# Performance work log

Hardware: AMD Instinct MI355X
Metric: run time of the kernel (lower is better)

## Reference

```python
import jax, jax.numpy as jnp
import numpy as np

B, S, D = 1024, 200, 128
NQ, NC, NQD, NCD = 50000, 1000, 101, 101


def _linear_params(k, fan_in, fan_out):
    bound = 1.0 / np.sqrt(fan_in)
    kw, kb = jax.random.split(k)
    W = jax.random.uniform(kw, (fan_out, fan_in), minval=-bound, maxval=bound, dtype=jnp.float32)
    b = jax.random.uniform(kb, (fan_out,), minval=-bound, maxval=bound, dtype=jnp.float32)
    return W, b


def setup_inputs() -> dict:
    key = jax.random.key(0)
    ks = jax.random.split(key, 17)
    Wx, bx = _linear_params(ks[0], 4 * D, D)
    Ws1, bs1 = _linear_params(ks[1], D, D)
    Ws2, bs2 = _linear_params(ks[2], D, D)
    Wp1, bp1 = _linear_params(ks[3], 2 * D, D)
    Wp2, bp2 = _linear_params(ks[4], 2 * D, D)
    Wk, bk = _linear_params(ks[5], 4 * D, D)
    Eq = jax.random.normal(ks[6], (NQ, D), dtype=jnp.float32)
    Ec = jax.random.normal(ks[7], (NC, D), dtype=jnp.float32)
    Eqd = jax.random.normal(ks[8], (NQD, D), dtype=jnp.float32)
    Ecd = jax.random.normal(ks[9], (NCD, D), dtype=jnp.float32)
    Ecorr = jax.random.normal(ks[10], (2, D), dtype=jnp.float32)
    # xavier_uniform init for h_pre (torch: gain*sqrt(6/(fan_in+fan_out)) on [B,D])
    bh = np.sqrt(6.0 / (B + D))
    h0 = jax.random.uniform(ks[11], (B, D), minval=-bh, maxval=bh, dtype=jnp.float32)
    question_seq = jax.random.randint(ks[12], (B, S), 0, NQ)
    concept_seq = jax.random.randint(ks[13], (B, S), 0, NC)
    question_diff_seq = jax.random.randint(ks[14], (B, S), 0, NQD)
    concept_diff_seq = jax.random.randint(ks[15], (B, S), 0, NCD)
    correct_seq = jax.random.randint(ks[16], (B, S), 0, 2)
    return dict(question_seq=question_seq, concept_seq=concept_seq,
                question_diff_seq=question_diff_seq, concept_diff_seq=concept_diff_seq,
                correct_seq=correct_seq,
                Eq=Eq, Ec=Ec, Eqd=Eqd, Ecd=Ecd, Ecorr=Ecorr,
                Wx=Wx, bx=bx, Ws1=Ws1, bs1=bs1, Ws2=Ws2, bs2=bs2,
                Wp1=Wp1, bp1=bp1, Wp2=Wp2, bp2=bp2, Wk=Wk, bk=bk, h0=h0)


def reference(question_seq, concept_seq, question_diff_seq, concept_diff_seq, correct_seq,
              Eq, Ec, Eqd, Ecd, Ecorr,
              Wx, bx, Ws1, bs1, Ws2, bs2, Wp1, bp1, Wp2, bp2, Wk, bk, h0):
    qe = Eq[question_seq]            # [B,S,D]
    ce = Ec[concept_seq]
    qde = Eqd[question_diff_seq]
    cde = Ecd[concept_diff_seq]
    corr = Ecorr[correct_seq]
    # generate_x_MLP applied to all timesteps at once (same math as per-step)
    x = jnp.concatenate([qe, ce, qde, cde], axis=-1) @ Wx.T + bx  # [B,S,D]
    # time-major inputs for the scan over t = 0 .. S-2
    xs = (jnp.swapaxes(x[:, :-1], 0, 1),      # x_t       [S-1,B,D]
          jnp.swapaxes(x[:, 1:], 0, 1),       # x_{t+1}
          jnp.swapaxes(corr[:, :-1], 0, 1),
          jnp.swapaxes(qde[:, :-1], 0, 1),
          jnp.swapaxes(cde[:, :-1], 0, 1))

    def step(h_pre, inp):
        xt, xnext, ct, qdt, cdt = inp
        s_in = xt - h_pre
        sdf = jax.nn.sigmoid(s_in @ Ws1.T + bs1) * jnp.tanh(s_in @ Ws2.T + bs2)  # dropout=eval identity
        p_in = jnp.concatenate([sdf, ct], axis=-1)
        pka = jax.nn.sigmoid(p_in @ Wp1.T + bp1) * jnp.tanh(p_in @ Wp2.T + bp2)
        k_in = jnp.concatenate([h_pre, ct, qdt, cdt], axis=-1)
        g = jax.nn.sigmoid(k_in @ Wk.T + bk)
        h = g * h_pre + (1.0 - g) * pka
        yt = jax.nn.sigmoid(jnp.sum(xnext * h, axis=-1))  # [B]
        return h, yt

    _, ys = jax.lax.scan(step, h0, xs)  # ys: [S-1,B]
    y = jnp.concatenate([ys.T, jnp.zeros((question_seq.shape[0], 1), x.dtype)], axis=1)  # [B,S], y[:, S-1]=0
    return y
```

## Files before the change

### kernel.cpp

```cpp
#include <hip/hip_runtime.h>
#include <hip/hip_bf16.h>


#define S_LEN 200
#define NBATCH 1024
#define DIM 128
#define LOG2E 1.4426950408889634f
#define NPROD 191

typedef short short8 __attribute__((ext_vector_type(8)));
typedef float f32x4 __attribute__((ext_vector_type(4)));

__device__ __forceinline__ unsigned short f2b(float f) {
  union { float f; unsigned u; } v; v.f = f;
  unsigned r = (v.u + 0x7FFFu + ((v.u >> 16) & 1u)) >> 16;
  return (unsigned short)r;
}
__device__ __forceinline__ float b2f(unsigned short b) {
  union { unsigned u; float f; } v; v.u = ((unsigned)b) << 16;
  return v.f;
}
__device__ __forceinline__ unsigned pk_bf16(float lo, float hi) {
  __hip_bfloat162 t = __float22bfloat162_rn(make_float2(lo, hi));
  union { __hip_bfloat162 h; unsigned u; } cv; cv.h = t;
  return cv.u;
}
__device__ __forceinline__ float fast_sigmoid(float x) {
  return __builtin_amdgcn_rcpf(1.0f + __builtin_amdgcn_exp2f(-LOG2E * x));
}
__device__ __forceinline__ float fast_tanh(float x) {
  return 2.0f * __builtin_amdgcn_rcpf(1.0f + __builtin_amdgcn_exp2f(-2.0f * LOG2E * x)) - 1.0f;
}
__device__ __forceinline__ void wg_barrier_lds() {
  __asm__ volatile("s_waitcnt lgkmcnt(0)\n\ts_barrier" ::: "memory");
}

__global__ void proj_all_kernel(const float* __restrict__ Eq, const float* __restrict__ Ec,
                                const float* __restrict__ Eqd, const float* __restrict__ Ecd,
                                const float* __restrict__ Ecorr,
                                const float* __restrict__ Wx,
                                const float* __restrict__ Wp1, const float* __restrict__ bp1,
                                const float* __restrict__ Wp2, const float* __restrict__ bp2,
                                const float* __restrict__ Wk, const float* __restrict__ bk,
                                unsigned short* __restrict__ Tq, unsigned short* __restrict__ Tc,
                                unsigned short* __restrict__ Tqd, unsigned short* __restrict__ Tcd,
                                unsigned short* __restrict__ Tkqd, unsigned short* __restrict__ Tkcd,
                                float* __restrict__ Tkc, float* __restrict__ Tp1c,
                                float* __restrict__ Tp2c, int* __restrict__ syncz) {
  const int bid = blockIdx.x;
  const int tid = threadIdx.x;
  if (bid >= 802) {
    const int blk = bid - 802;
    if (blk < 101) {
      const int o = tid & 127, half = tid >> 7;
      const float* e = (half ? Ecd : Eqd) + (size_t)blk * DIM;
      const float* wr = Wk + (size_t)o * 512 + (half ? 384 : 256);
      float a = 0.f;
      for (int k = 0; k < DIM; ++k) a = fmaf(e[k], wr[k], a);
      (half ? Tkcd : Tkqd)[blk * DIM + o] = f2b(a);
    } else {
      for (int idx = tid; idx < 768; idx += 256) {
        const int t = idx >> 8, e = (idx >> 7) & 1, o = idx & 127;
        const float* ec = Ecorr + e * DIM;
        const float* wr; float bias; float* dst;
        if (t == 0)      { wr = Wp1 + (size_t)o * 256 + 128; bias = bp1[o]; dst = Tp1c; }
        else if (t == 1) { wr = Wp2 + (size_t)o * 256 + 128; bias = bp2[o]; dst = Tp2c; }
        else             { wr = Wk  + (size_t)o * 512 + 128; bias = bk[o];  dst = Tkc;  }
        float a = bias;
        for (int k = 0; k < DIM; ++k) a = fmaf(ec[k], wr[k], a);
        dst[e * DIM + o] = a;
      }
      for (int i2 = tid; i2 < 272; i2 += 256) syncz[i2] = 0;
    }
    return;
  }
  const float* E; int M, coff, r0; unsigned short* T;
  if (bid < 782)      { E = Eq;  M = 50000; coff = 0;   T = Tq;  r0 = bid * 64; }
  else if (bid < 798) { E = Ec;  M = 1000;  coff = 128; T = Tc;  r0 = (bid - 782) * 64; }
  else if (bid < 800) { E = Eqd; M = 101;   coff = 256; T = Tqd; r0 = (bid - 798) * 64; }
  else                { E = Ecd; M = 101;   coff = 384; T = Tcd; r0 = (bid - 800) * 64; }

  __shared__ __align__(16) unsigned short A[64][136];
  {
    const int row = tid >> 2, cb = (tid & 3) * 32;
    union U8 { uint4 v; unsigned short s[8]; } o;
#pragma unroll
    for (int cc = 0; cc < 4; ++cc) {
      const int c8 = cb + cc * 8;
      if (r0 + row < M) {
        const float4 e0 = *(const float4*)(E + (size_t)(r0 + row) * DIM + c8);
        const float4 e1 = *(const float4*)(E + (size_t)(r0 + row) * DIM + c8 + 4);
        o.s[0] = f2b(e0.x); o.s[1] = f2b(e0.y); o.s[2] = f2b(e0.z); o.s[3] = f2b(e0.w);
        o.s[4] = f2b(e1.x); o.s[5] = f2b(e1.y); o.s[6] = f2b(e1.z); o.s[7] = f2b(e1.w);
      } else {
        o.v = make_uint4(0, 0, 0, 0);
      }
      *(uint4*)&A[row][c8] = o.v;
    }
  }
  __syncthreads();
  const int w = tid >> 6, L = tid & 63, q = L >> 4, m = L & 15;
  short8 bf[2][4];
#pragma unroll
  for (int T2 = 0; T2 < 2; ++T2) {
    const int n = 32 * w + 16 * T2 + m;
#pragma unroll
    for (int kb = 0; kb < 4; ++kb) {
      const float* src = Wx + (size_t)n * 512 + coff + kb * 32 + q * 8;
      const float4 v0 = *(const float4*)src;
      const float4 v1 = *(const float4*)(src + 4);
      short8 f;
      f[0] = (short)f2b(v0.x); f[1] = (short)f2b(v0.y);
      f[2] = (short)f2b(v0.z); f[3] = (short)f2b(v0.w);
      f[4] = (short)f2b(v1.x); f[5] = (short)f2b(v1.y);
      f[6] = (short)f2b(v1.z); f[7] = (short)f2b(v1.w);
      bf[T2][kb] = f;
    }
  }
  const f32x4 vzero = {0.f, 0.f, 0.f, 0.f};
#pragma unroll
  for (int mt = 0; mt < 4; ++mt) {
    short8 af[4];
#pragma unroll
    for (int kb = 0; kb < 4; ++kb) af[kb] = *(const short8*)&A[mt * 16 + m][kb * 32 + q * 8];
    f32x4 acc[2] = {vzero, vzero};
#pragma unroll
    for (int kb = 0; kb < 4; ++kb) {
#pragma unroll
      for (int T2 = 0; T2 < 2; ++T2)
        acc[T2] = __builtin_amdgcn_mfma_f32_16x16x32_bf16(af[kb], bf[T2][kb], acc[T2], 0, 0, 0);
    }
#pragma unroll
    for (int T2 = 0; T2 < 2; ++T2) {
      const int col = 32 * w + 16 * T2 + m;
#pragma unroll
      for (int i = 0; i < 4; ++i) {
        const int r = r0 + mt * 16 + q * 4 + i;
        if (r < M) T[(size_t)r * DIM + col] = f2b(acc[T2][i]);
      }
    }
  }
}

__global__ void build_x_kernel(const int* __restrict__ qs, const int* __restrict__ cs,
                               const int* __restrict__ qds, const int* __restrict__ cds,
                               const int* __restrict__ corr,
                               const unsigned short* __restrict__ Tq, const unsigned short* __restrict__ Tc,
                               const unsigned short* __restrict__ Tqd, const unsigned short* __restrict__ Tcd,
                               const float* __restrict__ bx, unsigned short* __restrict__ xg,
                               float* __restrict__ SSg, float* __restrict__ corrf) {
  const int r = blockIdx.x * 16 + (threadIdx.x >> 4);
  const int c8 = (threadIdx.x & 15) * 8;
  const int s = r >> 10, b = r & 1023;
  const int q = qs[b * S_LEN + s], c = cs[b * S_LEN + s];
  const int qd = qds[b * S_LEN + s], cd = cds[b * S_LEN + s];
  union U8 { uint4 v; unsigned short s[8]; };
  U8 vq, vc, vd, ve, o;
  vq.v = *(const uint4*)(Tq + (size_t)q * DIM + c8);
  vc.v = *(const uint4*)(Tc + (size_t)c * DIM + c8);
  vd.v = *(const uint4*)(Tqd + (size_t)qd * DIM + c8);
  ve.v = *(const uint4*)(Tcd + (size_t)cd * DIM + c8);
  const float4 bx0 = *(const float4*)(bx + c8);
  const float4 bx1 = *(const float4*)(bx + c8 + 4);
  float bb[8] = {bx0.x, bx0.y, bx0.z, bx0.w, bx1.x, bx1.y, bx1.z, bx1.w};
  float part = 0.f;
#pragma unroll
  for (int j = 0; j < 8; ++j) {
    const float sv = b2f(vq.s[j]) + b2f(vc.s[j]) + b2f(vd.s[j]) + b2f(ve.s[j]) + bb[j];
    o.s[j] = f2b(sv);
    const float xr = b2f(o.s[j]);
    part = fmaf(xr, xr, part);
  }
  *(uint4*)(xg + (size_t)r * DIM + c8) = o.v;
#pragma unroll
  for (int off = 1; off <= 8; off <<= 1) part += __shfl_xor(part, off, 64);
  if ((threadIdx.x & 15) == 0) {
    SSg[r] = part;
    corrf[r] = (float)corr[b * S_LEN + s];
  }
}

__global__ void gemm_xg_kernel(const unsigned short* __restrict__ xg,
                               const float* __restrict__ Wk,
                               const int* __restrict__ corr, const int* __restrict__ qds,
                               const int* __restrict__ cds,
                               const float* __restrict__ Tkc,
                               const unsigned short* __restrict__ Tkqd,
                               const unsigned short* __restrict__ Tkcd,
                               unsigned short* __restrict__ GG) {
  const int tid = threadIdx.x;
  const int r0 = blockIdx.x * 64;
  __shared__ __align__(16) unsigned short TS[64][136];
  {
    const int row = tid >> 2, cb = (tid & 3) * 32;
    const int r = r0 + row, t = r >> 10, b = r & 1023;
    const int ci = corr[b * S_LEN + t], qi = qds[b * S_LEN + t], di = cds[b * S_LEN + t];
    union U8 { uint4 v; unsigned short s[8]; };
#pragma unroll
    for (int cc = 0; cc < 4; ++cc) {
      const int c8 = cb + cc * 8;
      U8 vq, vc, o;
      vq.v = *(const uint4*)(Tkqd + (size_t)qi * DIM + c8);
      vc.v = *(const uint4*)(Tkcd + (size_t)di * DIM + c8);
      const float4 k0 = *(const float4*)(Tkc + (size_t)ci * DIM + c8);
      const float4 k1 = *(const float4*)(Tkc + (size_t)ci * DIM + c8 + 4);
      float kk[8] = {k0.x, k0.y, k0.z, k0.w, k1.x, k1.y, k1.z, k1.w};
#pragma unroll
      for (int j = 0; j < 8; ++j) o.s[j] = f2b(kk[j] + b2f(vq.s[j]) + b2f(vc.s[j]));
      *(uint4*)&TS[row][c8] = o.v;
    }
  }
  __syncthreads();
  const int w = tid >> 6, L = tid & 63, q = L >> 4, m = L & 15;
  short8 wk[2][4];
#pragma unroll
  for (int T = 0; T < 2; ++T) {
    const int n = 32 * w + 16 * T + m;
#pragma unroll
    for (int kb = 0; kb < 4; ++kb) {
      const float* src = Wk + (size_t)n * 512 + kb * 32 + q * 8;
      const float4 v0 = *(const float4*)src;
      const float4 v1 = *(const float4*)(src + 4);
      short8 f;
      f[0] = (short)f2b(v0.x); f[1] = (short)f2b(v0.y);
      f[2] = (short)f2b(v0.z); f[3] = (short)f2b(v0.w);
      f[4] = (short)f2b(v1.x); f[5] = (short)f2b(v1.y);
      f[6] = (short)f2b(v1.z); f[7] = (short)f2b(v1.w);
      wk[T][kb] = f;
    }
  }
  const f32x4 vzero = {0.f, 0.f, 0.f, 0.f};
#pragma unroll
  for (int mt = 0; mt < 4; ++mt) {
    short8 af[4];
#pragma unroll
    for (int kb = 0; kb < 4; ++kb)
      af[kb] = *(const short8*)(xg + (size_t)(r0 + mt * 16 + m) * DIM + kb * 32 + q * 8);
    f32x4 acc[2] = {vzero, vzero};
#pragma unroll
    for (int kb = 0; kb < 4; ++kb) {
#pragma unroll
      for (int T = 0; T < 2; ++T)
        acc[T] = __builtin_amdgcn_mfma_f32_16x16x32_bf16(af[kb], wk[T][kb], acc[T], 0, 0, 0);
    }
#pragma unroll
    for (int T = 0; T < 2; ++T) {
      const int col = 32 * w + 16 * T + m;
#pragma unroll
      for (int i = 0; i < 4; ++i) {
        const int row64 = mt * 16 + q * 4 + i;
        GG[(size_t)(r0 + row64) * DIM + col] = f2b(acc[T][i] + b2f(TS[row64][col]));
      }
    }
  }
}

__device__ __forceinline__ void producer_body(
    const int p,
    const int* __restrict__ qs, const int* __restrict__ cs,
    const int* __restrict__ qds, const int* __restrict__ cds,
    const int* __restrict__ corr,
    const unsigned short* __restrict__ Tq, const unsigned short* __restrict__ Tc,
    const unsigned short* __restrict__ Tqd, const unsigned short* __restrict__ Tcd,
    const float* __restrict__ bx, const float* __restrict__ Wk,
    const float* __restrict__ Tkc, const unsigned short* __restrict__ Tkqd,
    const unsigned short* __restrict__ Tkcd,
    unsigned short* __restrict__ X, unsigned short* __restrict__ GG,
    float* __restrict__ SSg, float* __restrict__ corrf,
    int* donecnt, unsigned short (*xtile)[136], unsigned short (*TS)[136]) {
  const int tid = threadIdx.x;
  const int w = tid >> 6, L = tid & 63, q = L >> 4, m = L & 15;
  const int n = 16 * w + m;
  short8 wk[4];
#pragma unroll
  for (int kb = 0; kb < 4; ++kb) {
    const float* src = Wk + (size_t)n * 512 + kb * 32 + q * 8;
    const float4 v0 = *(const float4*)src;
    const float4 v1 = *(const float4*)(src + 4);
    short8 f;
    f[0] = (short)f2b(v0.x); f[1] = (short)f2b(v0.y);
    f[2] = (short)f2b(v0.z); f[3] = (short)f2b(v0.w);
    f[4] = (short)f2b(v1.x); f[5] = (short)f2b(v1.y);
    f[6] = (short)f2b(v1.z); f[7] = (short)f2b(v1.w);
    wk[kb] = f;
  }
  const int row = tid >> 3, k8 = tid & 7;
  const int c0 = k8 * 16;
  float bxv[16];
#pragma unroll
  for (int j = 0; j < 4; ++j) {
    const float4 bv = *(const float4*)(bx + c0 + j * 4);
    bxv[4 * j + 0] = bv.x; bxv[4 * j + 1] = bv.y;
    bxv[4 * j + 2] = bv.z; bxv[4 * j + 3] = bv.w;
  }
  const f32x4 vzero = {0.f, 0.f, 0.f, 0.f};
  union U8 { uint4 v; unsigned short s[8]; };

  for (int i = p; i < 3200; i += NPROD) {
    const int t = i >> 4, c = i & 15;
    const int b = c * 64 + row;
    const int base = b * S_LEN + t;
    const int qi = qs[base], ci = cs[base], qdi = qds[base], cdi = cds[base], cri = corr[base];
    float part = 0.f;
#pragma unroll
    for (int jj = 0; jj < 2; ++jj) {
      const int c8 = c0 + jj * 8;
      U8 vq, vc, vd, ve, o;
      vq.v = *(const uint4*)(Tq + (size_t)qi * DIM + c8);
      vc.v = *(const uint4*)(Tc + (size_t)ci * DIM + c8);
      vd.v = *(const uint4*)(Tqd + (size_t)qdi * DIM + c8);
      ve.v = *(const uint4*)(Tcd + (size_t)cdi * DIM + c8);
#pragma unroll
      for (int j = 0; j < 8; ++j) {
        const float sv = b2f(vq.s[j]) + b2f(vc.s[j]) + b2f(vd.s[j]) + b2f(ve.s[j]) + bxv[jj * 8 + j];
        o.s[j] = f2b(sv);
        const float xr = b2f(o.s[j]);
        part = fmaf(xr, xr, part);
      }
      *(uint4*)&xtile[row][c8] = o.v;
      *(uint4*)(X + (size_t)(t * 1024 + b) * DIM + c8) = o.v;
    }
#pragma unroll
    for (int off2 = 1; off2 <= 4; off2 <<= 1) part += __shfl_xor(part, off2, 64);
    if (k8 == 0) {
      SSg[t * 1024 + b] = part;
      corrf[t * 1024 + b] = (float)cri;
    }
    if (t < 199) {
#pragma unroll
      for (int jj = 0; jj < 2; ++jj) {
        const int c8 = c0 + jj * 8;
        U8 vq, vc, o;
        vq.v = *(const uint4*)(Tkqd + (size_t)qdi * DIM + c8);
        vc.v = *(const uint4*)(Tkcd + (size_t)cdi * DIM + c8);
        const float4 k0 = *(const float4*)(Tkc + (size_t)cri * DIM + c8);
        const float4 k1 = *(const float4*)(Tkc + (size_t)cri * DIM + c8 + 4);
        float kk[8] = {k0.x, k0.y, k0.z, k0.w, k1.x, k1.y, k1.z, k1.w};
#pragma unroll
        for (int j = 0; j < 8; ++j) o.s[j] = f2b(kk[j] + b2f(vq.s[j]) + b2f(vc.s[j]));
        *(uint4*)&TS[row][c8] = o.v;
      }
    }
    __syncthreads();
    if (t < 199) {
#pragma unroll
      for (int mt = 0; mt < 4; ++mt) {
        short8 af[4];
#pragma unroll
        for (int kb = 0; kb < 4; ++kb) af[kb] = *(const short8*)&xtile[mt * 16 + m][kb * 32 + q * 8];
        f32x4 acc = vzero;
#pragma unroll
        for (int kb = 0; kb < 4; ++kb)
          acc = __builtin_amdgcn_mfma_f32_16x16x32_bf16(af[kb], wk[kb], acc, 0, 0, 0);
#pragma unroll
        for (int i2 = 0; i2 < 4; ++i2) {
          const int row64 = mt * 16 + q * 4 + i2;
          GG[(size_t)(t * 1024 + c * 64 + row64) * DIM + n] = f2b(acc[i2] + b2f(TS[row64][n]));
        }
      }
    }
    __syncthreads();
    if (tid == 0)
      __hip_atomic_fetch_add(donecnt + t, 1, __ATOMIC_RELEASE, __HIP_MEMORY_SCOPE_AGENT);
  }
}

template <bool PIPE>
__device__ __forceinline__ void scan_body(
    const unsigned short* __restrict__ xg, const unsigned short* __restrict__ gg,
    const float* __restrict__ SSg, const float* __restrict__ corrf,
    const float* __restrict__ h0,
    const float* __restrict__ Ws1, const float* __restrict__ bs1,
    const float* __restrict__ Ws2, const float* __restrict__ bs2,
    const float* __restrict__ Wp1, const float* __restrict__ Wp2,
    const float* __restrict__ Wk,
    const float* __restrict__ gTp1c, const float* __restrict__ gTp2c,
    float* __restrict__ outp, int* wmp, unsigned short* ldsbase) {
  unsigned short (*Sbuf)[136] = (unsigned short (*)[136])ldsbase;
  unsigned short (*Pbuf)[136] = (unsigned short (*)[136])(ldsbase + 16 * 136);

  const int tid = threadIdx.x;
  const int w = tid >> 6, L = tid & 63, q = L >> 4, m = L & 15;
  const int col16 = 16 * w + m;
  const int rbase = blockIdx.x << 4;
  const size_t SB = (size_t)NBATCH * DIM;

  short8 wf[5][4];
  {
    const float* Wptr[5] = {Ws1, Ws2, Wp1, Wp2, Wk};
    const int ldw[5] = {128, 128, 256, 256, 512};
#pragma unroll
    for (int M = 0; M < 5; ++M) {
#pragma unroll
      for (int kb = 0; kb < 4; ++kb) {
        const float* src = Wptr[M] + (size_t)col16 * ldw[M] + kb * 32 + q * 8;
        const float4 v0 = *(const float4*)src;
        const float4 v1 = *(const float4*)(src + 4);
        short8 f;
        f[0] = (short)f2b(v0.x); f[1] = (short)f2b(v0.y);
        f[2] = (short)f2b(v0.z); f[3] = (short)f2b(v0.w);
        f[4] = (short)f2b(v1.x); f[5] = (short)f2b(v1.y);
        f[6] = (short)f2b(v1.z); f[7] = (short)f2b(v1.w);
        wf[M][kb] = f;
      }
    }
  }
  const float bs1v = bs1[col16], bs2v = bs2[col16];
  const float tp1v0 = gTp1c[col16], dtp1 = gTp1c[DIM + col16] - tp1v0;
  const float tp2v0 = gTp2c[col16], dtp2 = gTp2c[DIM + col16] - tp2v0;
  if (tid < 16) outp[(size_t)(rbase + tid) * S_LEN + (S_LEN - 1)] = 0.0f;

  int wm_seen = 0;
  auto wait_wm = [&](int need) {
    if (wm_seen >= need) return;
    while (__hip_atomic_load(wmp, __ATOMIC_RELAXED, __HIP_MEMORY_SCOPE_AGENT) < need)
      __builtin_amdgcn_s_sleep(8);
    wm_seen = __hip_atomic_load(wmp, __ATOMIC_ACQUIRE, __HIP_MEMORY_SCOPE_AGENT);
  };
  if (PIPE) wait_wm(3);

  float h[4];
#pragma unroll
  for (int i = 0; i < 4; ++i) {
    const int b = rbase + q * 4 + i;
    const float hv = h0[(size_t)b * DIM + col16];
    h[i] = hv;
    const float xt = b2f(xg[(size_t)b * DIM + col16]);
    Sbuf[q * 4 + i][col16] = f2b(xt - hv);
  }
  float* poy = outp + (size_t)(rbase + m) * S_LEN;

  unsigned short XPA[4], XPB[4], GPA[4], GPB[4];
  float4 CFA, CFB;
  short8 XFA[4], XFB[4];
  float SSA, SSB;
  const unsigned short* pxA = xg + 3 * SB + (size_t)(rbase + q * 4) * DIM + col16;
  const unsigned short* pxB = pxA + SB;
  const unsigned short* pgA = gg + 2 * SB + (size_t)(rbase + q * 4) * DIM + col16;
  const unsigned short* pgB = pgA + SB;
  const float* pcA = corrf + 2 * NBATCH + rbase + q * 4;
  const float* pcB = pcA + NBATCH;
  const unsigned short* pfA = xg + 2 * SB + (size_t)(rbase + m) * DIM + q * 8;
  const unsigned short* pfB = pfA + SB;
  const float* psA = SSg + 2 * NBATCH + rbase + m;
  const float* psB = psA + NBATCH;
#pragma unroll
  for (int i = 0; i < 4; ++i) {
    XPA[i] = xg[SB + (size_t)(rbase + q * 4 + i) * DIM + col16];
    XPB[i] = xg[2 * SB + (size_t)(rbase + q * 4 + i) * DIM + col16];
    GPA[i] = gg[(size_t)(rbase + q * 4 + i) * DIM + col16];
    GPB[i] = gg[SB + (size_t)(rbase + q * 4 + i) * DIM + col16];
  }
  CFA = *(const float4*)(corrf + rbase + q * 4);
  CFB = *(const float4*)(corrf + NBATCH + rbase + q * 4);
#pragma unroll
  for (int kb = 0; kb < 4; ++kb) {
    XFA[kb] = *(const short8*)(xg + (size_t)(rbase + m) * DIM + kb * 32 + q * 8);
    XFB[kb] = *(const short8*)(xg + SB + (size_t)(rbase + m) * DIM + kb * 32 + q * 8);
  }
  SSA = SSg[rbase + m];
  SSB = SSg[NBATCH + rbase + m];

  const f32x4 vzero = {0.f, 0.f, 0.f, 0.f};

#define STEP(TCUR, XP, GP, CF, PX, PG, PC, XF, SSR, PF, PS)                    \
  do {                                                                         \
    const int t_ = (TCUR);                                                     \
    float xnv[4], ggv[4], cfv[4];                                              \
    _Pragma("unroll") for (int i = 0; i < 4; ++i) {                            \
      xnv[i] = b2f(XP[i]); ggv[i] = b2f(GP[i]);                                \
    }                                                                          \
    cfv[0] = CF.x; cfv[1] = CF.y; cfv[2] = CF.z; cfv[3] = CF.w;                \
    short8 xfr[4]; float ssv = SSR;                                            \
    if (w == 0) {                                                              \
      _Pragma("unroll") for (int kb = 0; kb < 4; ++kb) xfr[kb] = XF[kb];       \
    }                                                                          \
    _Pragma("unroll") for (int i = 0; i < 4; ++i) {                            \
      XP[i] = PX[i * DIM]; GP[i] = PG[i * DIM];                                \
    }                                                                          \
    CF = *(const float4*)PC;                                                   \
    PX += 2 * SB; PG += 2 * SB; PC += 2 * NBATCH;                              \
    if (w == 0) {                                                              \
      _Pragma("unroll") for (int kb = 0; kb < 4; ++kb)                         \
        XF[kb] = *(const short8*)(PF + kb * 32);                               \
      SSR = *PS;                                                               \
      PF += 2 * SB; PS += 2 * NBATCH;                                          \
    }                                                                          \
    wg_barrier_lds();                                       \
    short8 sf[4];                                                              \
    _Pragma("unroll") for (int kb = 0; kb < 4; ++kb)                           \
        sf[kb] = *(const short8*)&Sbuf[m][kb * 32 + q * 8];                    \
    f32x4 a1 = vzero, a2 = vzero, c1 = vzero;                                  \
    _Pragma("unroll") for (int kb = 0; kb < 4; ++kb) {                         \
      a1 = __builtin_amdgcn_mfma_f32_16x16x32_bf16(sf[kb], wf[0][kb], a1, 0, 0, 0); \
      a2 = __builtin_amdgcn_mfma_f32_16x16x32_bf16(sf[kb], wf[1][kb], a2, 0, 0, 0); \
      c1 = __builtin_amdgcn_mfma_f32_16x16x32_bf16(sf[kb], wf[4][kb], c1, 0, 0, 0); \
    }                                                                          \
    if (w == 0) {                                                              \
      f32x4 dt = vzero;                                                        \
      _Pragma("unroll") for (int kb = 0; kb < 4; ++kb)                         \
        dt = __builtin_amdgcn_mfma_f32_16x16x32_bf16(sf[kb], xfr[kb], dt, 0, 0, 0); \
      if (t_ > 0 && q == (m >> 2)) {                                           \
        const int ii = m & 3;                                                  \
        const float D = ii == 0 ? dt[0] : ii == 1 ? dt[1] : ii == 2 ? dt[2] : dt[3]; \
        poy[t_ - 1] = fast_sigmoid(ssv - D);                                   \
      }                                                                        \
    }                                                                          \
    _Pragma("unroll") for (int i2 = 0; i2 < 2; ++i2) {                         \
      const float s0 = fast_sigmoid(a1[2 * i2] + bs1v) * fast_tanh(a2[2 * i2] + bs2v); \
      const float s1 = fast_sigmoid(a1[2 * i2 + 1] + bs1v) * fast_tanh(a2[2 * i2 + 1] + bs2v); \
      const unsigned u = pk_bf16(s0, s1);                                      \
      Pbuf[q * 4 + 2 * i2][col16] = (unsigned short)u;                         \
      Pbuf[q * 4 + 2 * i2 + 1][col16] = (unsigned short)(u >> 16);             \
    }                                                                          \
    wg_barrier_lds();                                          \
    short8 pf[4];                                                              \
    _Pragma("unroll") for (int kb = 0; kb < 4; ++kb)                           \
        pf[kb] = *(const short8*)&Pbuf[m][kb * 32 + q * 8];                    \
    f32x4 p1 = vzero, p2 = vzero;                                              \
    _Pragma("unroll") for (int kb = 0; kb < 4; ++kb) {                         \
      p1 = __builtin_amdgcn_mfma_f32_16x16x32_bf16(pf[kb], wf[2][kb], p1, 0, 0, 0); \
      p2 = __builtin_amdgcn_mfma_f32_16x16x32_bf16(pf[kb], wf[3][kb], p2, 0, 0, 0); \
    }                                                                          \
    float sn[4];                                                               \
    _Pragma("unroll") for (int i = 0; i < 4; ++i) {                            \
      const float g = fast_sigmoid(ggv[i] - c1[i]);                            \
      const float t1v = fmaf(cfv[i], dtp1, tp1v0);                             \
      const float t2v = fmaf(cfv[i], dtp2, tp2v0);                             \
      const float pka = fast_sigmoid(p1[i] + t1v) * fast_tanh(p2[i] + t2v);    \
      const float hn = pka + g * (h[i] - pka);                                 \
      h[i] = hn;                                                               \
      sn[i] = xnv[i] - hn;                                                     \
    }                                                                          \
    _Pragma("unroll") for (int i2 = 0; i2 < 2; ++i2) {                         \
      const unsigned u = pk_bf16(sn[2 * i2], sn[2 * i2 + 1]);                  \
      Sbuf[q * 4 + 2 * i2][col16] = (unsigned short)u;                         \
      Sbuf[q * 4 + 2 * i2 + 1][col16] = (unsigned short)(u >> 16);             \
    }                                                                          \
  } while (0)

  for (int t2 = 0; t2 < 198; t2 += 2) {
    if (PIPE) {
      const int need = (t2 + 5 > 200) ? 200 : t2 + 5;
      wait_wm(need);
    }
    STEP(t2, XPA, GPA, CFA, pxA, pgA, pcA, XFA, SSA, pfA, psA);
    STEP(t2 + 1, XPB, GPB, CFB, pxB, pgB, pcB, XFB, SSB, pfB, psB);
  }
  STEP(198, XPA, GPA, CFA, pxA, pgA, pcA, XFA, SSA, pfA, psA);
#undef STEP

  wg_barrier_lds();
  if (w == 0) {
    short8 sf[4];
#pragma unroll
    for (int kb = 0; kb < 4; ++kb) sf[kb] = *(const short8*)&Sbuf[m][kb * 32 + q * 8];
    f32x4 dt = vzero;
#pragma unroll
    for (int kb = 0; kb < 4; ++kb)
      dt = __builtin_amdgcn_mfma_f32_16x16x32_bf16(sf[kb], XFB[kb], dt, 0, 0, 0);
    if (q == (m >> 2)) {
      const int ii = m & 3;
      const float D = ii == 0 ? dt[0] : ii == 1 ? dt[1] : ii == 2 ? dt[2] : dt[3];
      poy[S_LEN - 2] = fast_sigmoid(SSB - D);
    }
  }
}

template <bool PIPE>
__global__ __launch_bounds__(512, 2) void scan_fused_kernel(
    const unsigned short* __restrict__ xg, const unsigned short* __restrict__ gg,
    const float* __restrict__ SSg, const float* __restrict__ corrf,
    const float* __restrict__ h0,
    const float* __restrict__ Ws1, const float* __restrict__ bs1,
    const float* __restrict__ Ws2, const float* __restrict__ bs2,
    const float* __restrict__ Wp1, const float* __restrict__ Wp2,
    const float* __restrict__ WkF,
    const float* __restrict__ gTp1c, const float* __restrict__ gTp2c,
    float* __restrict__ outp,
    const int* __restrict__ qs, const int* __restrict__ cs,
    const int* __restrict__ qds, const int* __restrict__ cds,
    const int* __restrict__ corr,
    const unsigned short* __restrict__ Tq, const unsigned short* __restrict__ Tc,
    const unsigned short* __restrict__ Tqd, const unsigned short* __restrict__ Tcd,
    const float* __restrict__ bx, const float* __restrict__ Tkc,
    const unsigned short* __restrict__ Tkqd, const unsigned short* __restrict__ Tkcd,
    unsigned short* __restrict__ Xw, unsigned short* __restrict__ GGw,
    float* __restrict__ SSw, float* __restrict__ corrw,
    int* donecnt, int* wmp) {
  __shared__ __align__(16) unsigned short lds[PIPE ? 2 * 64 * 136 : 2 * 16 * 136];
  if (!PIPE || blockIdx.x < 64) {
    scan_body<PIPE>(xg, gg, SSg, corrf, h0, Ws1, bs1, Ws2, bs2, Wp1, Wp2, WkF,
                    gTp1c, gTp2c, outp, wmp, lds);
    return;
  }
  if constexpr (PIPE) {
    if (blockIdx.x == 255) {
      if (threadIdx.x == 0) {
        for (int t = 0; t < S_LEN; ++t) {
          while (__hip_atomic_load(donecnt + t, __ATOMIC_RELAXED, __HIP_MEMORY_SCOPE_AGENT) < 16)
            __builtin_amdgcn_s_sleep(8);
          (void)__hip_atomic_load(donecnt + t, __ATOMIC_ACQUIRE, __HIP_MEMORY_SCOPE_AGENT);
          __hip_atomic_store(wmp, t + 1, __ATOMIC_RELEASE, __HIP_MEMORY_SCOPE_AGENT);
        }
      }
      return;
    }
    producer_body(blockIdx.x - 64, qs, cs, qds, cds, corr, Tq, Tc, Tqd, Tcd, bx,
                  WkF, Tkc, Tkqd, Tkcd, Xw, GGw, SSw, corrw, donecnt,
                  (unsigned short (*)[136])lds,
                  (unsigned short (*)[136])(lds + 64 * 136));
  }
}

extern "C" void kernel_launch(void* const* d_in, const int* in_sizes, int n_in,
                              void* d_out, int out_size, void* d_ws, size_t ws_size,
                              hipStream_t stream) {
  const int* qs    = (const int*)d_in[0];
  const int* cs    = (const int*)d_in[1];
  const int* qds   = (const int*)d_in[2];
  const int* cds   = (const int*)d_in[3];
  const int* corr  = (const int*)d_in[4];
  const float* Eq    = (const float*)d_in[5];
  const float* Ec    = (const float*)d_in[6];
  const float* Eqd   = (const float*)d_in[7];
  const float* Ecd   = (const float*)d_in[8];
  const float* Ecorr = (const float*)d_in[9];
  const float* Wx  = (const float*)d_in[10];
  const float* bx  = (const float*)d_in[11];
  const float* Ws1 = (const float*)d_in[12];
  const float* bs1 = (const float*)d_in[13];
  const float* Ws2 = (const float*)d_in[14];
  const float* bs2 = (const float*)d_in[15];
  const float* Wp1 = (const float*)d_in[16];
  const float* bp1 = (const float*)d_in[17];
  const float* Wp2 = (const float*)d_in[18];
  const float* bp2 = (const float*)d_in[19];
  const float* Wk  = (const float*)d_in[20];
  const float* bk  = (const float*)d_in[21];
  const float* h0  = (const float*)d_in[22];

  char* ws = (char*)d_ws;
  const size_t xbytes = (size_t)S_LEN * NBATCH * DIM * 2;
  const size_t ggbytes = (size_t)(S_LEN - 1) * NBATCH * DIM * 2;

  {
    size_t off = 0;
    auto alloc = [&](size_t bytes) {
      void* p = ws + off;
      off = (off + bytes + 255) & ~(size_t)255;
      return p;
    };
    unsigned short* X  = (unsigned short*)alloc(xbytes);
    unsigned short* GG = (unsigned short*)alloc(ggbytes);
    float* corrf = (float*)alloc((size_t)S_LEN * NBATCH * 4);
    float* SS    = (float*)alloc((size_t)S_LEN * NBATCH * 4);
    unsigned short* Tq  = (unsigned short*)alloc((size_t)50000 * DIM * 2);
    unsigned short* Tc  = (unsigned short*)alloc((size_t)1000 * DIM * 2);
    unsigned short* Tqd = (unsigned short*)alloc((size_t)101 * DIM * 2);
    unsigned short* Tcd = (unsigned short*)alloc((size_t)101 * DIM * 2);
    unsigned short* Tkqd = (unsigned short*)alloc((size_t)101 * DIM * 2);
    unsigned short* Tkcd = (unsigned short*)alloc((size_t)101 * DIM * 2);
    float* Tkc  = (float*)alloc((size_t)2 * DIM * 4);
    float* Tp1c = (float*)alloc((size_t)2 * DIM * 4);
    float* Tp2c = (float*)alloc((size_t)2 * DIM * 4);
    int* syncz  = (int*)alloc(2048);
    if (off <= ws_size) {
      proj_all_kernel<<<904, 256, 0, stream>>>(Eq, Ec, Eqd, Ecd, Ecorr, Wx,
                                               Wp1, bp1, Wp2, bp2, Wk, bk,
                                               Tq, Tc, Tqd, Tcd, Tkqd, Tkcd,
                                               Tkc, Tp1c, Tp2c, syncz);
      scan_fused_kernel<true><<<256, 512, 0, stream>>>(
          X, GG, SS, corrf, h0, Ws1, bs1, Ws2, bs2, Wp1, Wp2, Wk, Tp1c, Tp2c,
          (float*)d_out, qs, cs, qds, cds, corr, Tq, Tc, Tqd, Tcd, bx,
          Tkc, Tkqd, Tkcd, X, GG, SS, corrf, syncz, syncz + 256);
      return;
    }
  }

  const size_t A = (xbytes + 255) & ~(size_t)255;
  unsigned short* X  = (unsigned short*)ws;
  unsigned short* GG = (unsigned short*)(ws + A);
  unsigned short* Tq  = GG;
  unsigned short* Tc  = (unsigned short*)(ws + A + (size_t)50000 * DIM * 2);
  unsigned short* Tqd = (unsigned short*)(ws + A + (size_t)51000 * DIM * 2);
  unsigned short* Tcd = (unsigned short*)(ws + A + (size_t)51101 * DIM * 2);
  size_t off = A + ((ggbytes + 255) & ~(size_t)255);
  auto alloc = [&](size_t bytes) {
    void* p = ws + off;
    off = (off + bytes + 255) & ~(size_t)255;
    return p;
  };
  float* corrf = (float*)alloc((size_t)S_LEN * NBATCH * 4);
  float* SS    = (float*)alloc((size_t)S_LEN * NBATCH * 4);
  unsigned short* Tkqd = (unsigned short*)alloc((size_t)101 * DIM * 2);
  unsigned short* Tkcd = (unsigned short*)alloc((size_t)101 * DIM * 2);
  float* Tkc  = (float*)alloc((size_t)2 * DIM * 4);
  float* Tp1c = (float*)alloc((size_t)2 * DIM * 4);
  float* Tp2c = (float*)alloc((size_t)2 * DIM * 4);
  int* syncz  = (int*)alloc(2048);

  proj_all_kernel<<<904, 256, 0, stream>>>(Eq, Ec, Eqd, Ecd, Ecorr, Wx,
                                           Wp1, bp1, Wp2, bp2, Wk, bk,
                                           Tq, Tc, Tqd, Tcd, Tkqd, Tkcd, Tkc, Tp1c, Tp2c,
                                           syncz);
  build_x_kernel<<<(S_LEN * NBATCH) / 16, 256, 0, stream>>>(qs, cs, qds, cds, corr,
                                                            Tq, Tc, Tqd, Tcd, bx, X, SS, corrf);
  gemm_xg_kernel<<<((S_LEN - 1) * NBATCH) / 64, 256, 0, stream>>>(X, Wk, corr, qds, cds,
                                                                  Tkc, Tkqd, Tkcd, GG);
  scan_fused_kernel<false><<<64, 512, 0, stream>>>(
      X, GG, SS, corrf, h0, Ws1, bs1, Ws2, bs2, Wp1, Wp2, Wk, Tp1c, Tp2c,
      (float*)d_out, qs, cs, qds, cds, corr, Tq, Tc, Tqd, Tcd, bx,
      Tkc, Tkqd, Tkcd, X, GG, SS, corrf, syncz, syncz + 256);
}
```

Baseline: 491.7 us.

## Fold embedding projection into persistent producer blocks and drop watermark block

Moves the embedding-table projection (Tq/Tc/Tqd/Tcd/Tkqd/Tkcd/Tkc) from a separate kernel into the 192 producer blocks of the fused scan kernel, followed by a grid-wide atomic barrier. Scan blocks compute the Ecorr-dependent Tp1c/Tp2c terms themselves, and poll per-timestep done counters directly instead of going through a dedicated watermark block. The intent is to remove a kernel launch boundary and let scan blocks start their setup while projection runs. In exchange, the projection work is spread over fewer blocks and adds a spin barrier, and a tiny zero-init kernel is still launched.

```diff
diff --git a/kernel.cpp b/kernel.cpp
--- a/kernel.cpp
+++ b/kernel.cpp
@@ -6,7 +6,8 @@
 #define NBATCH 1024
 #define DIM 128
 #define LOG2E 1.4426950408889634f
-#define NPROD 191
+#define NPROD 192
+#define NCHUNK 854
 
 typedef short short8 __attribute__((ext_vector_type(8)));
 typedef float f32x4 __attribute__((ext_vector_type(4)));
@@ -34,6 +35,8 @@
 __device__ __forceinline__ void wg_barrier_lds() {
   __asm__ volatile("s_waitcnt lgkmcnt(0)\n\ts_barrier" ::: "memory");
 }
+
+__global__ void zero_sync_kernel(int* __restrict__ s) { s[threadIdx.x] = 0; }
 
 __global__ void proj_all_kernel(const float* __restrict__ Eq, const float* __restrict__ Ec,
                                 const float* __restrict__ Eqd, const float* __restrict__ Ecd,
@@ -46,7 +49,7 @@
                                 unsigned short* __restrict__ Tqd, unsigned short* __restrict__ Tcd,
                                 unsigned short* __restrict__ Tkqd, unsigned short* __restrict__ Tkcd,
                                 float* __restrict__ Tkc, float* __restrict__ Tp1c,
-                                float* __restrict__ Tp2c, int* __restrict__ syncz) {
+                                float* __restrict__ Tp2c) {
   const int bid = blockIdx.x;
   const int tid = threadIdx.x;
   if (bid >= 802) {
@@ -70,7 +73,6 @@
         for (int k = 0; k < DIM; ++k) a = fmaf(ec[k], wr[k], a);
         dst[e * DIM + o] = a;
       }
-      for (int i2 = tid; i2 < 272; i2 += 256) syncz[i2] = 0;
     }
     return;
   }
@@ -255,20 +257,114 @@
   }
 }
 
+__device__ __forceinline__ void proj_chunk(
+    const int j, const int tid,
+    const float* Eq, const float* Ec, const float* Eqd, const float* Ecd,
+    const float* Ecorr, const float* Wx, const float* Wk, const float* bk,
+    unsigned short* Tq, unsigned short* Tc, unsigned short* Tqd, unsigned short* Tcd,
+    float* Tkc, unsigned short* Tkqd, unsigned short* Tkcd,
+    unsigned short (*A)[136]) {
+  if (j < 802) {
+    const float* E; int M, coff, r0; unsigned short* T;
+    if (j < 782)      { E = Eq;  M = 50000; coff = 0;   T = Tq;  r0 = j * 64; }
+    else if (j < 798) { E = Ec;  M = 1000;  coff = 128; T = Tc;  r0 = (j - 782) * 64; }
+    else if (j < 800) { E = Eqd; M = 101;   coff = 256; T = Tqd; r0 = (j - 798) * 64; }
+    else              { E = Ecd; M = 101;   coff = 384; T = Tcd; r0 = (j - 800) * 64; }
+    {
+      const int row = tid >> 3, c0 = (tid & 7) * 16;
+      union U8 { uint4 v; unsigned short s[8]; } o;
+#pragma unroll
+      for (int cc = 0; cc < 2; ++cc) {
+        const int c8 = c0 + cc * 8;
+        if (r0 + row < M) {
+          const float4 e0 = *(const float4*)(E + (size_t)(r0 + row) * DIM + c8);
+          const float4 e1 = *(const float4*)(E + (size_t)(r0 + row) * DIM + c8 + 4);
+          o.s[0] = f2b(e0.x); o.s[1] = f2b(e0.y); o.s[2] = f2b(e0.z); o.s[3] = f2b(e0.w);
+          o.s[4] = f2b(e1.x); o.s[5] = f2b(e1.y); o.s[6] = f2b(e1.z); o.s[7] = f2b(e1.w);
+        } else {
+          o.v = make_uint4(0, 0, 0, 0);
+        }
+        *(uint4*)&A[row][c8] = o.v;
+      }
+    }
+    __syncthreads();
+    const int w = tid >> 6, L = tid & 63, q = L >> 4, m = L & 15;
+    const int n = 16 * w + m;
+    short8 bf[4];
+#pragma unroll
+    for (int kb = 0; kb < 4; ++kb) {
+      const float* src = Wx + (size_t)n * 512 + coff + kb * 32 + q * 8;
+      const float4 v0 = *(const float4*)src;
+      const float4 v1 = *(const float4*)(src + 4);
+      short8 f;
+      f[0] = (short)f2b(v0.x); f[1] = (short)f2b(v0.y);
+      f[2] = (short)f2b(v0.z); f[3] = (short)f2b(v0.w);
+      f[4] = (short)f2b(v1.x); f[5] = (short)f2b(v1.y);
+      f[6] = (short)f2b(v1.z); f[7] = (short)f2b(v1.w);
+      bf[kb] = f;
+    }
+    const f32x4 vzero = {0.f, 0.f, 0.f, 0.f};
+#pragma unroll
+    for (int mt = 0; mt < 4; ++mt) {
+      short8 af[4];
+#pragma unroll
+      for (int kb = 0; kb < 4; ++kb) af[kb] = *(const short8*)&A[mt * 16 + m][kb * 32 + q * 8];
+      f32x4 acc = vzero;
+#pragma unroll
+      for (int kb = 0; kb < 4; ++kb)
+        acc = __builtin_amdgcn_mfma_f32_16x16x32_bf16(af[kb], bf[kb], acc, 0, 0, 0);
+#pragma unroll
+      for (int i = 0; i < 4; ++i) {
+        const int r = r0 + mt * 16 + q * 4 + i;
+        if (r < M) T[(size_t)r * DIM + n] = f2b(acc[i]);
+      }
+    }
+    __syncthreads();
+  } else if (j < 853) {
+    const int blk = 2 * (j - 802) + ((tid >> 8) & 1);
+    const int o = tid & 127, half = (tid >> 7) & 1;
+    if (blk < 101) {
+      const float* e = (half ? Ecd : Eqd) + (size_t)blk * DIM;
+      const float* wr = Wk + (size_t)o * 512 + (half ? 384 : 256);
+      float a = 0.f;
+      for (int k = 0; k < DIM; ++k) a = fmaf(e[k], wr[k], a);
+      (half ? Tkcd : Tkqd)[blk * DIM + o] = f2b(a);
+    }
+  } else {
+    if (tid < 256) {
+      const int e2 = tid >> 7, o = tid & 127;
+      const float* ec = Ecorr + e2 * DIM;
+      const float* wr = Wk + (size_t)o * 512 + 128;
+      float a = bk[o];
+      for (int k = 0; k < DIM; ++k) a = fmaf(ec[k], wr[k], a);
+      Tkc[e2 * DIM + o] = a;
+    }
+  }
+}
+
 __device__ __forceinline__ void producer_body(
     const int p,
-    const int* __restrict__ qs, const int* __restrict__ cs,
-    const int* __restrict__ qds, const int* __restrict__ cds,
-    const int* __restrict__ corr,
-    const unsigned short* __restrict__ Tq, const unsigned short* __restrict__ Tc,
-    const unsigned short* __restrict__ Tqd, const unsigned short* __restrict__ Tcd,
-    const float* __restrict__ bx, const float* __restrict__ Wk,
-    const float* __restrict__ Tkc, const unsigned short* __restrict__ Tkqd,
-    const unsigned short* __restrict__ Tkcd,
-    unsigned short* __restrict__ X, unsigned short* __restrict__ GG,
-    float* __restrict__ SSg, float* __restrict__ corrf,
-    int* donecnt, unsigned short (*xtile)[136], unsigned short (*TS)[136]) {
+    const int* qs, const int* cs, const int* qds, const int* cds, const int* corr,
+    const float* Eq, const float* Ec, const float* Eqd, const float* Ecd,
+    const float* Ecorr, const float* Wx, const float* bk,
+    unsigned short* Tq, unsigned short* Tc, unsigned short* Tqd, unsigned short* Tcd,
+    const float* bx, const float* Wk,
+    float* Tkc, unsigned short* Tkqd, unsigned short* Tkcd,
+    unsigned short* X, unsigned short* GG, float* SSg, float* corrf,
+    int* donecnt, int* projdone,
+    unsigned short (*xtile)[136], unsigned short (*TS)[136]) {
   const int tid = threadIdx.x;
+
+  for (int j = p; j < NCHUNK; j += NPROD)
+    proj_chunk(j, tid, Eq, Ec, Eqd, Ecd, Ecorr, Wx, Wk, bk,
+               Tq, Tc, Tqd, Tcd, Tkc, Tkqd, Tkcd, xtile);
+  __syncthreads();
+  if (tid == 0)
+    __hip_atomic_fetch_add(projdone, 1, __ATOMIC_RELEASE, __HIP_MEMORY_SCOPE_AGENT);
+  while (__hip_atomic_load(projdone, __ATOMIC_RELAXED, __HIP_MEMORY_SCOPE_AGENT) < NPROD)
+    __builtin_amdgcn_s_sleep(4);
+  (void)__hip_atomic_load(projdone, __ATOMIC_ACQUIRE, __HIP_MEMORY_SCOPE_AGENT);
+
   const int w = tid >> 6, L = tid & 63, q = L >> 4, m = L & 15;
   const int n = 16 * w + m;
   short8 wk[4];
@@ -372,10 +468,10 @@
     const float* __restrict__ h0,
     const float* __restrict__ Ws1, const float* __restrict__ bs1,
     const float* __restrict__ Ws2, const float* __restrict__ bs2,
-    const float* __restrict__ Wp1, const float* __restrict__ Wp2,
-    const float* __restrict__ Wk,
-    const float* __restrict__ gTp1c, const float* __restrict__ gTp2c,
-    float* __restrict__ outp, int* wmp, unsigned short* ldsbase) {
+    const float* __restrict__ Wp1, const float* __restrict__ bp1,
+    const float* __restrict__ Wp2, const float* __restrict__ bp2,
+    const float* __restrict__ Wk, const float* __restrict__ Ecorr,
+    float* __restrict__ outp, int* dc, unsigned short* ldsbase) {
   unsigned short (*Sbuf)[136] = (unsigned short (*)[136])ldsbase;
   unsigned short (*Pbuf)[136] = (unsigned short (*)[136])(ldsbase + 16 * 136);
 
@@ -406,18 +502,43 @@
     }
   }
   const float bs1v = bs1[col16], bs2v = bs2[col16];
-  const float tp1v0 = gTp1c[col16], dtp1 = gTp1c[DIM + col16] - tp1v0;
-  const float tp2v0 = gTp2c[col16], dtp2 = gTp2c[DIM + col16] - tp2v0;
+  float tp1v0, dtp1, tp2v0, dtp2;
+  {
+    float t10 = bp1[col16], t11 = t10;
+    float t20 = bp2[col16], t21 = t20;
+    const float* w1r = Wp1 + (size_t)col16 * 256 + 128;
+    const float* w2r = Wp2 + (size_t)col16 * 256 + 128;
+    for (int k = 0; k < DIM; k += 4) {
+      const float4 a0 = *(const float4*)(Ecorr + k);
+      const float4 a1 = *(const float4*)(Ecorr + DIM + k);
+      const float4 b1 = *(const float4*)(w1r + k);
+      const float4 b2 = *(const float4*)(w2r + k);
+      t10 = fmaf(a0.x, b1.x, t10); t10 = fmaf(a0.y, b1.y, t10);
+      t10 = fmaf(a0.z, b1.z, t10); t10 = fmaf(a0.w, b1.w, t10);
+      t11 = fmaf(a1.x, b1.x, t11); t11 = fmaf(a1.y, b1.y, t11);
+      t11 = fmaf(a1.z, b1.z, t11); t11 = fmaf(a1.w, b1.w, t11);
+      t20 = fmaf(a0.x, b2.x, t20); t20 = fmaf(a0.y, b2.y, t20);
+      t20 = fmaf(a0.z, b2.z, t20); t20 = fmaf(a0.w, b2.w, t20);
+      t21 = fmaf(a1.x, b2.x, t21); t21 = fmaf(a1.y, b2.y, t21);
+      t21 = fmaf(a1.z, b2.z, t21); t21 = fmaf(a1.w, b2.w, t21);
+    }
+    tp1v0 = t10; dtp1 = t11 - t10;
+    tp2v0 = t20; dtp2 = t21 - t20;
+  }
   if (tid < 16) outp[(size_t)(rbase + tid) * S_LEN + (S_LEN - 1)] = 0.0f;
 
-  int wm_seen = 0;
-  auto wait_wm = [&](int need) {
-    if (wm_seen >= need) return;
-    while (__hip_atomic_load(wmp, __ATOMIC_RELAXED, __HIP_MEMORY_SCOPE_AGENT) < need)
-      __builtin_amdgcn_s_sleep(8);
-    wm_seen = __hip_atomic_load(wmp, __ATOMIC_ACQUIRE, __HIP_MEMORY_SCOPE_AGENT);
+  int done_upto = 0;
+  auto wait_t = [&](int need) {
+    while (done_upto < need) {
+      if (__hip_atomic_load(dc + done_upto, __ATOMIC_RELAXED, __HIP_MEMORY_SCOPE_AGENT) >= 16) {
+        (void)__hip_atomic_load(dc + done_upto, __ATOMIC_ACQUIRE, __HIP_MEMORY_SCOPE_AGENT);
+        ++done_upto;
+      } else {
+        __builtin_amdgcn_s_sleep(2);
+      }
+    }
   };
-  if (PIPE) wait_wm(3);
+  if (PIPE) wait_t(3);
 
   float h[4];
 #pragma unroll
@@ -542,7 +663,7 @@
   for (int t2 = 0; t2 < 198; t2 += 2) {
     if (PIPE) {
       const int need = (t2 + 5 > 200) ? 200 : t2 + 5;
-      wait_wm(need);
+      wait_t(need);
     }
     STEP(t2, XPA, GPA, CFA, pxA, pgA, pcA, XFA, SSA, pfA, psA);
     STEP(t2 + 1, XPB, GPB, CFB, pxB, pgB, pcB, XFB, SSB, pfB, psB);
@@ -569,45 +690,29 @@
 
 template <bool PIPE>
 __global__ __launch_bounds__(512, 2) void scan_fused_kernel(
-    const unsigned short* __restrict__ xg, const unsigned short* __restrict__ gg,
-    const float* __restrict__ SSg, const float* __restrict__ corrf,
-    const float* __restrict__ h0,
-    const float* __restrict__ Ws1, const float* __restrict__ bs1,
-    const float* __restrict__ Ws2, const float* __restrict__ bs2,
-    const float* __restrict__ Wp1, const float* __restrict__ Wp2,
-    const float* __restrict__ WkF,
-    const float* __restrict__ gTp1c, const float* __restrict__ gTp2c,
-    float* __restrict__ outp,
-    const int* __restrict__ qs, const int* __restrict__ cs,
-    const int* __restrict__ qds, const int* __restrict__ cds,
-    const int* __restrict__ corr,
-    const unsigned short* __restrict__ Tq, const unsigned short* __restrict__ Tc,
-    const unsigned short* __restrict__ Tqd, const unsigned short* __restrict__ Tcd,
-    const float* __restrict__ bx, const float* __restrict__ Tkc,
-    const unsigned short* __restrict__ Tkqd, const unsigned short* __restrict__ Tkcd,
-    unsigned short* __restrict__ Xw, unsigned short* __restrict__ GGw,
-    float* __restrict__ SSw, float* __restrict__ corrw,
-    int* donecnt, int* wmp) {
+    const unsigned short* xg, const unsigned short* gg,
+    const float* SSg, const float* corrf, const float* h0,
+    const float* Ws1, const float* bs1, const float* Ws2, const float* bs2,
+    const float* Wp1, const float* bp1, const float* Wp2, const float* bp2,
+    const float* WkF, const float* Ecorr, float* outp,
+    const int* qs, const int* cs, const int* qds, const int* cds, const int* corr,
+    unsigned short* Tq, unsigned short* Tc, unsigned short* Tqd, unsigned short* Tcd,
+    const float* bx, float* Tkc, unsigned short* Tkqd, unsigned short* Tkcd,
+    const float* Eq, const float* Ec, const float* Eqd, const float* Ecd,
+    const float* Wx, const float* bk,
+    unsigned short* Xw, unsigned short* GGw, float* SSw, float* corrw,
+    int* donecnt, int* projdone) {
   __shared__ __align__(16) unsigned short lds[PIPE ? 2 * 64 * 136 : 2 * 16 * 136];
   if (!PIPE || blockIdx.x < 64) {
-    scan_body<PIPE>(xg, gg, SSg, corrf, h0, Ws1, bs1, Ws2, bs2, Wp1, Wp2, WkF,
-                    gTp1c, gTp2c, outp, wmp, lds);
+    scan_body<PIPE>(xg, gg, SSg, corrf, h0, Ws1, bs1, Ws2, bs2, Wp1, bp1, Wp2, bp2,
+                    WkF, Ecorr, outp, donecnt, lds);
     return;
   }
   if constexpr (PIPE) {
-    if (blockIdx.x == 255) {
-      if (threadIdx.x == 0) {
-        for (int t = 0; t < S_LEN; ++t) {
-          while (__hip_atomic_load(donecnt + t, __ATOMIC_RELAXED, __HIP_MEMORY_SCOPE_AGENT) < 16)
-            __builtin_amdgcn_s_sleep(8);
-          (void)__hip_atomic_load(donecnt + t, __ATOMIC_ACQUIRE, __HIP_MEMORY_SCOPE_AGENT);
-          __hip_atomic_store(wmp, t + 1, __ATOMIC_RELEASE, __HIP_MEMORY_SCOPE_AGENT);
-        }
-      }
-      return;
-    }
-    producer_body(blockIdx.x - 64, qs, cs, qds, cds, corr, Tq, Tc, Tqd, Tcd, bx,
-                  WkF, Tkc, Tkqd, Tkcd, Xw, GGw, SSw, corrw, donecnt,
+    producer_body(blockIdx.x - 64, qs, cs, qds, cds, corr,
+                  Eq, Ec, Eqd, Ecd, Ecorr, Wx, bk,
+                  Tq, Tc, Tqd, Tcd, bx, WkF, Tkc, Tkqd, Tkcd,
+                  Xw, GGw, SSw, corrw, donecnt, projdone,
                   (unsigned short (*)[136])lds,
                   (unsigned short (*)[136])(lds + 64 * 136));
   }
@@ -662,18 +767,14 @@
     unsigned short* Tkqd = (unsigned short*)alloc((size_t)101 * DIM * 2);
     unsigned short* Tkcd = (unsigned short*)alloc((size_t)101 * DIM * 2);
     float* Tkc  = (float*)alloc((size_t)2 * DIM * 4);
-    float* Tp1c = (float*)alloc((size_t)2 * DIM * 4);
-    float* Tp2c = (float*)alloc((size_t)2 * DIM * 4);
     int* syncz  = (int*)alloc(2048);
     if (off <= ws_size) {
-      proj_all_kernel<<<904, 256, 0, stream>>>(Eq, Ec, Eqd, Ecd, Ecorr, Wx,
-                                               Wp1, bp1, Wp2, bp2, Wk, bk,
-                                               Tq, Tc, Tqd, Tcd, Tkqd, Tkcd,
-                                               Tkc, Tp1c, Tp2c, syncz);
+      zero_sync_kernel<<<1, 512, 0, stream>>>(syncz);
       scan_fused_kernel<true><<<256, 512, 0, stream>>>(
-          X, GG, SS, corrf, h0, Ws1, bs1, Ws2, bs2, Wp1, Wp2, Wk, Tp1c, Tp2c,
+          X, GG, SS, corrf, h0, Ws1, bs1, Ws2, bs2, Wp1, bp1, Wp2, bp2, Wk, Ecorr,
           (float*)d_out, qs, cs, qds, cds, corr, Tq, Tc, Tqd, Tcd, bx,
-          Tkc, Tkqd, Tkcd, X, GG, SS, corrf, syncz, syncz + 256);
+          Tkc, Tkqd, Tkcd, Eq, Ec, Eqd, Ecd, Wx, bk,
+          X, GG, SS, corrf, syncz, syncz + 256);
       return;
     }
   }
@@ -702,14 +803,14 @@
 
   proj_all_kernel<<<904, 256, 0, stream>>>(Eq, Ec, Eqd, Ecd, Ecorr, Wx,
                                            Wp1, bp1, Wp2, bp2, Wk, bk,
-                                           Tq, Tc, Tqd, Tcd, Tkqd, Tkcd, Tkc, Tp1c, Tp2c,
-                                           syncz);
+                                           Tq, Tc, Tqd, Tcd, Tkqd, Tkcd, Tkc, Tp1c, Tp2c);
   build_x_kernel<<<(S_LEN * NBATCH) / 16, 256, 0, stream>>>(qs, cs, qds, cds, corr,
                                                             Tq, Tc, Tqd, Tcd, bx, X, SS, corrf);
   gemm_xg_kernel<<<((S_LEN - 1) * NBATCH) / 64, 256, 0, stream>>>(X, Wk, corr, qds, cds,
                                                                   Tkc, Tkqd, Tkcd, GG);
   scan_fused_kernel<false><<<64, 512, 0, stream>>>(
-      X, GG, SS, corrf, h0, Ws1, bs1, Ws2, bs2, Wp1, Wp2, Wk, Tp1c, Tp2c,
+      X, GG, SS, corrf, h0, Ws1, bs1, Ws2, bs2, Wp1, bp1, Wp2, bp2, Wk, Ecorr,
       (float*)d_out, qs, cs, qds, cds, corr, Tq, Tc, Tqd, Tcd, bx,
-      Tkc, Tkqd, Tkcd, X, GG, SS, corrf, syncz, syncz + 256);
-}
+      Tkc, Tkqd, Tkcd, Eq, Ec, Eqd, Ecd, Wx, bk,
+      X, GG, SS, corrf, syncz, syncz + 256);
+}
```

Result: slower. 1.077 ms (+119.1%).
